# Kernel optimization log

Measured on AMD Instinct MI355X. Metric: run time of the kernel, lower is better.

The kernel has to match this reference:

```python
import jax, jax.numpy as jnp
import numpy as np

D_IN = 1024
D_OUT = 1024
NUM_HEADS = 16
HEAD_DIM = D_OUT // NUM_HEADS


def setup_inputs() -> dict:
    key = jax.random.key(0)
    ks = jax.random.split(key, 6)
    s = 0.02
    x = jax.random.normal(ks[0], (4, 2048, D_IN), dtype=jnp.float32)
    # nn.Linear weights are [out, in]
    Wq = jax.random.normal(ks[1], (D_OUT, D_IN), dtype=jnp.float32) * s
    Wk = jax.random.normal(ks[2], (D_OUT, D_IN), dtype=jnp.float32) * s
    Wv = jax.random.normal(ks[3], (D_OUT, D_IN), dtype=jnp.float32) * s
    Wo = jax.random.normal(ks[4], (D_OUT, D_OUT), dtype=jnp.float32) * s
    bo = jax.random.normal(ks[5], (D_OUT,), dtype=jnp.float32) * s
    return {"x": x, "Wq": Wq, "Wk": Wk, "Wv": Wv, "Wo": Wo, "bo": bo}


def reference(x, Wq, Wk, Wv, Wo, bo):
    B, T, _ = x.shape
    # project and split heads: [B, H, T, hd]
    def proj(W):
        return (x @ W.T).reshape(B, T, NUM_HEADS, HEAD_DIM).transpose(0, 2, 1, 3)
    q, k, v = proj(Wq), proj(Wk), proj(Wv)
    scores = jnp.einsum('bhqd,bhkd->bhqk', q, k) / jnp.sqrt(jnp.float32(HEAD_DIM))
    causal = jnp.tril(jnp.ones((T, T), dtype=bool))  # True = keep
    scores = jnp.where(causal, scores, -jnp.inf)
    attn = jax.nn.softmax(scores, axis=-1)
    ctx = jnp.einsum('bhqk,bhkd->bhqd', attn, v)  # [B,H,T,hd]
    ctx = ctx.transpose(0, 2, 1, 3).reshape(B, T, D_OUT)
    return ctx @ Wo.T + bo
```

## Files before the change

kernel.cpp:

```cpp
#include <hip/hip_runtime.h>

#define NH 16
#define HD 64
#define TSEQ 2048
#define DMODEL 1024

typedef __attribute__((ext_vector_type(8))) short short8;
typedef __attribute__((ext_vector_type(4))) float f32x4;

static __device__ __forceinline__ unsigned short f2bf(float f) {
    unsigned u = __builtin_bit_cast(unsigned, f);
    u += 0x7FFF + ((u >> 16) & 1);
    return (unsigned short)(u >> 16);
}

static __device__ __forceinline__ unsigned pk2(float a, float b) {
    unsigned ua = __builtin_bit_cast(unsigned, a);
    unsigned ub = __builtin_bit_cast(unsigned, b);
    return ((ua + 0x8000u) >> 16) | (((ub + 0x8000u) >> 16) << 16);
}

__global__ __launch_bounds__(256) void cast_f32_bf16(const float* __restrict__ src,
                                                     unsigned short* __restrict__ dst, int n4) {
    int i = blockIdx.x * 256 + threadIdx.x;
    if (i >= n4) return;
    float4 v = reinterpret_cast<const float4*>(src)[i];
    ushort4 o;
    o.x = f2bf(v.x); o.y = f2bf(v.y); o.z = f2bf(v.z); o.w = f2bf(v.w);
    reinterpret_cast<ushort4*>(dst)[i] = o;
}

static __device__ __forceinline__ void gemm_mainloop(const unsigned short* __restrict__ A,
                                                     const unsigned short* __restrict__ Bt,
                                                     int m0, int n0, int K,
                                                     unsigned short* As, unsigned short* Bs,
                                                     f32x4 acc[4][4]) {
    const int tid = threadIdx.x;
    const int lane = tid & 63;
    const int w = tid >> 6;
    const int wr = w >> 1, wc = w & 1;
    const int lrow = lane >> 2;
    const int lcol = (lane & 3) * 8;

    f32x4 zero = {0.f, 0.f, 0.f, 0.f};
#pragma unroll
    for (int i = 0; i < 4; i++)
#pragma unroll
        for (int j = 0; j < 4; j++) acc[i][j] = zero;

    for (int k0 = 0; k0 < K; k0 += 32) {
        __syncthreads();
#pragma unroll
        for (int c = w; c < 8; c += 4) {
            int row = c * 16 + lrow;
            __builtin_amdgcn_global_load_lds(
                (const __attribute__((address_space(1))) void*)(A + (size_t)(m0 + row) * K + k0 + lcol),
                (__attribute__((address_space(3))) void*)(As + c * 512), 16, 0, 0);
            __builtin_amdgcn_global_load_lds(
                (const __attribute__((address_space(1))) void*)(Bt + (size_t)(n0 + row) * K + k0 + lcol),
                (__attribute__((address_space(3))) void*)(Bs + c * 512), 16, 0, 0);
        }
        __syncthreads();

        const int ko = (lane >> 4) * 8;
        short8 a[4], b[4];
#pragma unroll
        for (int i = 0; i < 4; i++)
            a[i] = *(const short8*)(As + (wr * 64 + i * 16 + (lane & 15)) * 32 + ko);
#pragma unroll
        for (int j = 0; j < 4; j++)
            b[j] = *(const short8*)(Bs + (wc * 64 + j * 16 + (lane & 15)) * 32 + ko);
#pragma unroll
        for (int i = 0; i < 4; i++)
#pragma unroll
            for (int j = 0; j < 4; j++)
                acc[i][j] = __builtin_amdgcn_mfma_f32_16x16x32_bf16(a[i], b[j], acc[i][j], 0, 0, 0);
    }
}

#define QSCALE 0.180336880f
__global__ __launch_bounds__(256) void gemm_qkv(const unsigned short* __restrict__ xb,
                                                const unsigned short* __restrict__ Wqb,
                                                const unsigned short* __restrict__ Wkb,
                                                const unsigned short* __restrict__ Wvb,
                                                unsigned short* __restrict__ Q,
                                                unsigned short* __restrict__ K,
                                                unsigned short* __restrict__ Vt) {
    __shared__ __attribute__((aligned(16))) unsigned short As[128 * 32];
    __shared__ __attribute__((aligned(16))) unsigned short Bs[128 * 32];
    const int m0 = blockIdx.x * 128;
    const int n0 = blockIdx.y * 128;
    const int z = blockIdx.z;
    const unsigned short* Bt = (z == 0) ? Wqb : ((z == 1) ? Wkb : Wvb);
    unsigned short* out = (z == 0) ? Q : ((z == 1) ? K : Vt);

    f32x4 acc[4][4];
    gemm_mainloop(xb, Bt, m0, n0, DMODEL, As, Bs, acc);

    const int tid = threadIdx.x, lane = tid & 63, w = tid >> 6;
    const int wr = w >> 1, wc = w & 1;
    const float sc = (z == 0) ? QSCALE : 1.0f;
#pragma unroll
    for (int i = 0; i < 4; i++)
#pragma unroll
        for (int j = 0; j < 4; j++)
#pragma unroll
            for (int r = 0; r < 4; r++) {
                int row = m0 + wr * 64 + i * 16 + (lane >> 4) * 4 + r;
                int col = n0 + wc * 64 + j * 16 + (lane & 15);
                int b = row >> 11, t = row & 2047;
                int h = col >> 6, d = col & 63;
                unsigned short v = f2bf(acc[i][j][r] * sc);
                if (z == 2)
                    out[(((size_t)(b * NH + h)) * HD + d) * TSEQ + t] = v;
                else
                    out[(((size_t)(b * NH + h)) * TSEQ + t) * HD + d] = v;
            }
}

__global__ __launch_bounds__(256) void gemm_out(const unsigned short* __restrict__ ctx,
                                                const unsigned short* __restrict__ Wob,
                                                const float* __restrict__ bo,
                                                float* __restrict__ out) {
    __shared__ __attribute__((aligned(16))) unsigned short As[128 * 32];
    __shared__ __attribute__((aligned(16))) unsigned short Bs[128 * 32];
    const int m0 = blockIdx.x * 128;
    const int n0 = blockIdx.y * 128;

    f32x4 acc[4][4];
    gemm_mainloop(ctx, Wob, m0, n0, DMODEL, As, Bs, acc);

    const int tid = threadIdx.x, lane = tid & 63, w = tid >> 6;
    const int wr = w >> 1, wc = w & 1;
#pragma unroll
    for (int i = 0; i < 4; i++)
#pragma unroll
        for (int j = 0; j < 4; j++)
#pragma unroll
            for (int r = 0; r < 4; r++) {
                int row = m0 + wr * 64 + i * 16 + (lane >> 4) * 4 + r;
                int col = n0 + wc * 64 + j * 16 + (lane & 15);
                out[(size_t)row * DMODEL + col] = acc[i][j][r] + bo[col];
            }
}

__global__ __launch_bounds__(256) void attn(const unsigned short* __restrict__ Qg,
                                            const unsigned short* __restrict__ Kg,
                                            const unsigned short* __restrict__ Vg,
                                            unsigned short* __restrict__ ctx) {
    __shared__ __attribute__((aligned(16))) unsigned short Ks[64][72];
    __shared__ __attribute__((aligned(16))) unsigned short Vs[64][72];
    __shared__ __attribute__((aligned(16))) unsigned short Pl[128][76];

    const int tid = threadIdx.x, lane = tid & 63, w = tid >> 6;
    const int wq = w * 32;
    const int lg = lane >> 4;
    const int ll = lane & 15;
    const int bh = blockIdx.x;
    const int q0 = (gridDim.y - 1 - blockIdx.y) * 128;
    const unsigned short* Qh = Qg + (size_t)bh * TSEQ * HD;
    const unsigned short* Kh = Kg + (size_t)bh * TSEQ * HD;
    const unsigned short* Vh = Vg + (size_t)bh * HD * TSEQ;

    short8 qf[2][2];
#pragma unroll
    for (int rb = 0; rb < 2; rb++)
#pragma unroll
        for (int ks = 0; ks < 2; ks++)
            qf[rb][ks] = *(const short8*)(Qh + (size_t)(q0 + wq + rb * 16 + ll) * HD + ks * 32 + lg * 8);

    float mrun[2] = {-1e30f, -1e30f}, lrun[2] = {0.f, 0.f};
    f32x4 zero = {0.f, 0.f, 0.f, 0.f};
    f32x4 o_t[2][4];
#pragma unroll
    for (int rb = 0; rb < 2; rb++)
#pragma unroll
        for (int db = 0; db < 4; db++) o_t[rb][db] = zero;

    const int sr = tid >> 3;
    const int sc = (tid & 7) * 8;
    short8 kreg0, kreg1, vreg0, vreg1;
    {
        kreg0 = *(const short8*)(Kh + (size_t)(sr) * HD + sc);
        kreg1 = *(const short8*)(Kh + (size_t)(sr + 32) * HD + sc);
        vreg0 = *(const short8*)(Vh + (size_t)sr * TSEQ + sc);
        vreg1 = *(const short8*)(Vh + (size_t)(sr + 32) * TSEQ + sc);
    }

    const int nkv = q0 / 64 + 2;
    for (int kt = 0; kt < nkv; kt++) {
        const int kv0 = kt * 64;
        __builtin_amdgcn_s_barrier();
        __builtin_amdgcn_sched_barrier(0);
        *(short8*)&Ks[sr][sc] = kreg0;
        *(short8*)&Ks[sr + 32][sc] = kreg1;
        *(short8*)&Vs[sr][sc] = vreg0;
        *(short8*)&Vs[sr + 32][sc] = vreg1;
        if (kt + 1 < nkv) {
            const int nv0 = kv0 + 64;
            kreg0 = *(const short8*)(Kh + (size_t)(nv0 + sr) * HD + sc);
            kreg1 = *(const short8*)(Kh + (size_t)(nv0 + sr + 32) * HD + sc);
            vreg0 = *(const short8*)(Vh + (size_t)sr * TSEQ + nv0 + sc);
            vreg1 = *(const short8*)(Vh + (size_t)(sr + 32) * TSEQ + nv0 + sc);
        }
        __builtin_amdgcn_sched_barrier(0);
        asm volatile("s_waitcnt lgkmcnt(0)" ::: "memory");
        __builtin_amdgcn_s_barrier();
        __builtin_amdgcn_sched_barrier(0);

        f32x4 st[2][4];
#pragma unroll
        for (int rb = 0; rb < 2; rb++)
#pragma unroll
            for (int cb = 0; cb < 4; cb++) st[rb][cb] = zero;
#pragma unroll
        for (int ks = 0; ks < 2; ks++) {
            short8 afrag[4];
#pragma unroll
            for (int cb = 0; cb < 4; cb++)
                afrag[cb] = *(const short8*)&Ks[cb * 16 + ll][ks * 32 + lg * 8];
#pragma unroll
            for (int rb = 0; rb < 2; rb++)
#pragma unroll
                for (int cb = 0; cb < 4; cb++)
                    st[rb][cb] = __builtin_amdgcn_mfma_f32_16x16x32_bf16(afrag[cb], qf[rb][ks], st[rb][cb], 0, 0, 0);
        }

        if (kv0 + 63 > q0) {
#pragma unroll
            for (int rb = 0; rb < 2; rb++)
#pragma unroll
                for (int cb = 0; cb < 4; cb++)
#pragma unroll
                    for (int r = 0; r < 4; r++) {
                        int kvl = cb * 16 + lg * 4 + r;
                        int ql = wq + rb * 16 + ll;
                        if (kv0 + kvl > q0 + ql) st[rb][cb][r] = -1e30f;
                    }
        }

        float mx[2];
#pragma unroll
        for (int rb = 0; rb < 2; rb++) {
            float a0 = fmaxf(fmaxf(st[rb][0][0], st[rb][0][1]), fmaxf(st[rb][0][2], st[rb][0][3]));
            float a1 = fmaxf(fmaxf(st[rb][1][0], st[rb][1][1]), fmaxf(st[rb][1][2], st[rb][1][3]));
            float a2 = fmaxf(fmaxf(st[rb][2][0], st[rb][2][1]), fmaxf(st[rb][2][2], st[rb][2][3]));
            float a3 = fmaxf(fmaxf(st[rb][3][0], st[rb][3][1]), fmaxf(st[rb][3][2], st[rb][3][3]));
            float m = fmaxf(fmaxf(a0, a1), fmaxf(a2, a3));
            m = fmaxf(m, __shfl_xor(m, 16));
            m = fmaxf(m, __shfl_xor(m, 32));
            mx[rb] = m;
        }
        float need = fmaxf(mx[0] - mrun[0], mx[1] - mrun[1]);
        if (__any(need > 8.f)) {
#pragma unroll
            for (int rb = 0; rb < 2; rb++) {
                float mold = mrun[rb];
                float mn = fmaxf(mold, mx[rb]);
                float rs = __builtin_amdgcn_exp2f(mold - mn);
                mrun[rb] = mn;
                lrun[rb] *= rs;
#pragma unroll
                for (int db = 0; db < 4; db++)
#pragma unroll
                    for (int r = 0; r < 4; r++) o_t[rb][db][r] *= rs;
            }
        }
#pragma unroll
        for (int rb = 0; rb < 2; rb++) {
            float sum = 0.f;
#pragma unroll
            for (int cb = 0; cb < 4; cb++) {
                float p0 = __builtin_amdgcn_exp2f(st[rb][cb][0] - mrun[rb]);
                float p1 = __builtin_amdgcn_exp2f(st[rb][cb][1] - mrun[rb]);
                float p2 = __builtin_amdgcn_exp2f(st[rb][cb][2] - mrun[rb]);
                float p3 = __builtin_amdgcn_exp2f(st[rb][cb][3] - mrun[rb]);
                sum += (p0 + p1) + (p2 + p3);
                uint2 pw;
                pw.x = pk2(p0, p1);
                pw.y = pk2(p2, p3);
                *(uint2*)&Pl[wq + rb * 16 + ll][cb * 16 + lg * 4] = pw;
            }
            sum += __shfl_xor(sum, 16);
            sum += __shfl_xor(sum, 32);
            lrun[rb] += sum;
        }
        asm volatile("s_waitcnt lgkmcnt(0)" ::: "memory");
        __builtin_amdgcn_sched_barrier(0);

#pragma unroll
        for (int ks = 0; ks < 2; ks++) {
            short8 pa[2], va[4];
#pragma unroll
            for (int rb = 0; rb < 2; rb++)
                pa[rb] = *(const short8*)&Pl[wq + rb * 16 + ll][ks * 32 + lg * 8];
#pragma unroll
            for (int db = 0; db < 4; db++)
                va[db] = *(const short8*)&Vs[db * 16 + ll][ks * 32 + lg * 8];
#pragma unroll
            for (int rb = 0; rb < 2; rb++)
#pragma unroll
                for (int db = 0; db < 4; db++)
                    o_t[rb][db] = __builtin_amdgcn_mfma_f32_16x16x32_bf16(va[db], pa[rb], o_t[rb][db], 0, 0, 0);
        }
    }

    const int b = bh >> 4, h = bh & 15;
#pragma unroll
    for (int rb = 0; rb < 2; rb++) {
        float linv = 1.f / lrun[rb];
#pragma unroll
        for (int db = 0; db < 4; db++) {
            float v0 = o_t[rb][db][0] * linv, v1 = o_t[rb][db][1] * linv;
            float v2 = o_t[rb][db][2] * linv, v3 = o_t[rb][db][3] * linv;
            uint2 pw;
            pw.x = pk2(v0, v1);
            pw.y = pk2(v2, v3);
            *(uint2*)&Pl[wq + rb * 16 + ll][db * 16 + lg * 4] = pw;
        }
    }
    asm volatile("s_waitcnt lgkmcnt(0)" ::: "memory");
    __builtin_amdgcn_sched_barrier(0);
#pragma unroll
    for (int rb = 0; rb < 2; rb++)
#pragma unroll
        for (int half = 0; half < 2; half++) {
            short8 v = *(const short8*)&Pl[wq + rb * 16 + ll][half * 32 + lg * 8];
            size_t row = (size_t)(b * TSEQ + q0 + wq + rb * 16 + ll);
            *(short8*)(ctx + (row * NH + h) * HD + half * 32 + lg * 8) = v;
        }
}

extern "C" void kernel_launch(void* const* d_in, const int* in_sizes, int n_in,
                              void* d_out, int out_size, void* d_ws, size_t ws_size,
                              hipStream_t stream) {
    const float* x  = (const float*)d_in[0];
    const float* Wq = (const float*)d_in[1];
    const float* Wk = (const float*)d_in[2];
    const float* Wv = (const float*)d_in[3];
    const float* Wo = (const float*)d_in[4];
    const float* bo = (const float*)d_in[5];
    float* out = (float*)d_out;

    char* ws = (char*)d_ws;
    unsigned short* xb   = (unsigned short*)(ws);
    unsigned short* Wqb  = (unsigned short*)(ws + 16777216);
    unsigned short* Wkb  = (unsigned short*)(ws + 18874368);
    unsigned short* Wvb  = (unsigned short*)(ws + 20971520);
    unsigned short* Wob  = (unsigned short*)(ws + 23068672);
    unsigned short* Qb   = (unsigned short*)(ws + 25165824);
    unsigned short* Kb   = (unsigned short*)(ws + 41943040);
    unsigned short* Vtb  = (unsigned short*)(ws + 58720256);
    unsigned short* ctxb = (unsigned short*)(ws + 75497472);

    cast_f32_bf16<<<8192, 256, 0, stream>>>(x, xb, 2097152);
    cast_f32_bf16<<<1024, 256, 0, stream>>>(Wq, Wqb, 262144);
    cast_f32_bf16<<<1024, 256, 0, stream>>>(Wk, Wkb, 262144);
    cast_f32_bf16<<<1024, 256, 0, stream>>>(Wv, Wvb, 262144);
    cast_f32_bf16<<<1024, 256, 0, stream>>>(Wo, Wob, 262144);

    gemm_qkv<<<dim3(64, 8, 3), 256, 0, stream>>>(xb, Wqb, Wkb, Wvb, Qb, Kb, Vtb);
    attn<<<dim3(64, 16), 256, 0, stream>>>(Qb, Kb, Vtb, ctxb);
    gemm_out<<<dim3(64, 8), 256, 0, stream>>>(ctxb, Wob, bo, out);
}
```

Baseline: 204.8 us.

## Double-buffer GEMM LDS tiles, fuse weight casts, use hardware bf16 pack

The GEMM main loop now double-buffers its LDS tiles, issuing the async global-to-LDS load for the next K slice before computing on the current one, which cuts one barrier per iteration. The four weight-cast launches become a single kernel. In attention, the software bf16 rounding is replaced with the v_cvt_pk_bf16_f32 instruction, and the QK^T MFMA loop is reordered so all K fragments load first. The price is double the LDS per GEMM block, which may lower occupancy, and there is a possible race if the async LDS writes for the next slice are not waited on before the barrier.

```diff
diff --git a/kernel.cpp b/kernel.cpp
--- a/kernel.cpp
+++ b/kernel.cpp
@@ -14,10 +14,10 @@
     return (unsigned short)(u >> 16);
 }
 
-static __device__ __forceinline__ unsigned pk2(float a, float b) {
-    unsigned ua = __builtin_bit_cast(unsigned, a);
-    unsigned ub = __builtin_bit_cast(unsigned, b);
-    return ((ua + 0x8000u) >> 16) | (((ub + 0x8000u) >> 16) << 16);
+static __device__ __forceinline__ unsigned cvtpk(float a, float b) {
+    unsigned r;
+    asm("v_cvt_pk_bf16_f32 %0, %1, %2" : "=v"(r) : "v"(a), "v"(b));
+    return r;
 }
 
 __global__ __launch_bounds__(256) void cast_f32_bf16(const float* __restrict__ src,
@@ -28,6 +28,24 @@
     ushort4 o;
     o.x = f2bf(v.x); o.y = f2bf(v.y); o.z = f2bf(v.z); o.w = f2bf(v.w);
     reinterpret_cast<ushort4*>(dst)[i] = o;
+}
+
+__global__ __launch_bounds__(256) void cast_weights(const float* __restrict__ Wq,
+                                                    const float* __restrict__ Wk,
+                                                    const float* __restrict__ Wv,
+                                                    const float* __restrict__ Wo,
+                                                    unsigned short* __restrict__ dq,
+                                                    unsigned short* __restrict__ dk,
+                                                    unsigned short* __restrict__ dv,
+                                                    unsigned short* __restrict__ dwo) {
+    int g = blockIdx.x >> 10;
+    int i = (blockIdx.x & 1023) * 256 + threadIdx.x;
+    const float* s = (g == 0) ? Wq : (g == 1) ? Wk : (g == 2) ? Wv : Wo;
+    unsigned short* d = (g == 0) ? dq : (g == 1) ? dk : (g == 2) ? dv : dwo;
+    float4 v = reinterpret_cast<const float4*>(s)[i];
+    ushort4 o;
+    o.x = f2bf(v.x); o.y = f2bf(v.y); o.z = f2bf(v.z); o.w = f2bf(v.w);
+    reinterpret_cast<ushort4*>(d)[i] = o;
 }
 
 static __device__ __forceinline__ void gemm_mainloop(const unsigned short* __restrict__ A,
@@ -48,33 +66,41 @@
 #pragma unroll
         for (int j = 0; j < 4; j++) acc[i][j] = zero;
 
-    for (int k0 = 0; k0 < K; k0 += 32) {
-        __syncthreads();
+    auto stage = [&](int k0, int buf) {
 #pragma unroll
         for (int c = w; c < 8; c += 4) {
             int row = c * 16 + lrow;
             __builtin_amdgcn_global_load_lds(
                 (const __attribute__((address_space(1))) void*)(A + (size_t)(m0 + row) * K + k0 + lcol),
-                (__attribute__((address_space(3))) void*)(As + c * 512), 16, 0, 0);
+                (__attribute__((address_space(3))) void*)(As + buf * 4096 + c * 512), 16, 0, 0);
             __builtin_amdgcn_global_load_lds(
                 (const __attribute__((address_space(1))) void*)(Bt + (size_t)(n0 + row) * K + k0 + lcol),
-                (__attribute__((address_space(3))) void*)(Bs + c * 512), 16, 0, 0);
-        }
-        __syncthreads();
-
+                (__attribute__((address_space(3))) void*)(Bs + buf * 4096 + c * 512), 16, 0, 0);
+        }
+    };
+
+    stage(0, 0);
+    __syncthreads();
+    int cur = 0;
+    for (int k0 = 0; k0 < K; k0 += 32) {
+        if (k0 + 32 < K) stage(k0 + 32, cur ^ 1);
+        const unsigned short* Ab = As + cur * 4096;
+        const unsigned short* Bb = Bs + cur * 4096;
         const int ko = (lane >> 4) * 8;
         short8 a[4], b[4];
 #pragma unroll
         for (int i = 0; i < 4; i++)
-            a[i] = *(const short8*)(As + (wr * 64 + i * 16 + (lane & 15)) * 32 + ko);
+            a[i] = *(const short8*)(Ab + (wr * 64 + i * 16 + (lane & 15)) * 32 + ko);
 #pragma unroll
         for (int j = 0; j < 4; j++)
-            b[j] = *(const short8*)(Bs + (wc * 64 + j * 16 + (lane & 15)) * 32 + ko);
+            b[j] = *(const short8*)(Bb + (wc * 64 + j * 16 + (lane & 15)) * 32 + ko);
 #pragma unroll
         for (int i = 0; i < 4; i++)
 #pragma unroll
             for (int j = 0; j < 4; j++)
                 acc[i][j] = __builtin_amdgcn_mfma_f32_16x16x32_bf16(a[i], b[j], acc[i][j], 0, 0, 0);
+        __syncthreads();
+        cur ^= 1;
     }
 }
 
@@ -86,8 +112,8 @@
                                                 unsigned short* __restrict__ Q,
                                                 unsigned short* __restrict__ K,
                                                 unsigned short* __restrict__ Vt) {
-    __shared__ __attribute__((aligned(16))) unsigned short As[128 * 32];
-    __shared__ __attribute__((aligned(16))) unsigned short Bs[128 * 32];
+    __shared__ __attribute__((aligned(16))) unsigned short As[2 * 128 * 32];
+    __shared__ __attribute__((aligned(16))) unsigned short Bs[2 * 128 * 32];
     const int m0 = blockIdx.x * 128;
     const int n0 = blockIdx.y * 128;
     const int z = blockIdx.z;
@@ -122,8 +148,8 @@
                                                 const unsigned short* __restrict__ Wob,
                                                 const float* __restrict__ bo,
                                                 float* __restrict__ out) {
-    __shared__ __attribute__((aligned(16))) unsigned short As[128 * 32];
-    __shared__ __attribute__((aligned(16))) unsigned short Bs[128 * 32];
+    __shared__ __attribute__((aligned(16))) unsigned short As[2 * 128 * 32];
+    __shared__ __attribute__((aligned(16))) unsigned short Bs[2 * 128 * 32];
     const int m0 = blockIdx.x * 128;
     const int n0 = blockIdx.y * 128;
 
@@ -170,12 +196,12 @@
             qf[rb][ks] = *(const short8*)(Qh + (size_t)(q0 + wq + rb * 16 + ll) * HD + ks * 32 + lg * 8);
 
     float mrun[2] = {-1e30f, -1e30f}, lrun[2] = {0.f, 0.f};
-    f32x4 zero = {0.f, 0.f, 0.f, 0.f};
+    const f32x4 zerov = {0.f, 0.f, 0.f, 0.f};
     f32x4 o_t[2][4];
 #pragma unroll
     for (int rb = 0; rb < 2; rb++)
 #pragma unroll
-        for (int db = 0; db < 4; db++) o_t[rb][db] = zero;
+        for (int db = 0; db < 4; db++) o_t[rb][db] = zerov;
 
     const int sr = tid >> 3;
     const int sc = (tid & 7) * 8;
@@ -208,23 +234,23 @@
         __builtin_amdgcn_s_barrier();
         __builtin_amdgcn_sched_barrier(0);
 
+        short8 af0[4], af1[4];
+#pragma unroll
+        for (int cb = 0; cb < 4; cb++) {
+            af0[cb] = *(const short8*)&Ks[cb * 16 + ll][lg * 8];
+            af1[cb] = *(const short8*)&Ks[cb * 16 + ll][32 + lg * 8];
+        }
         f32x4 st[2][4];
 #pragma unroll
         for (int rb = 0; rb < 2; rb++)
 #pragma unroll
-            for (int cb = 0; cb < 4; cb++) st[rb][cb] = zero;
-#pragma unroll
-        for (int ks = 0; ks < 2; ks++) {
-            short8 afrag[4];
-#pragma unroll
             for (int cb = 0; cb < 4; cb++)
-                afrag[cb] = *(const short8*)&Ks[cb * 16 + ll][ks * 32 + lg * 8];
-#pragma unroll
-            for (int rb = 0; rb < 2; rb++)
-#pragma unroll
-                for (int cb = 0; cb < 4; cb++)
-                    st[rb][cb] = __builtin_amdgcn_mfma_f32_16x16x32_bf16(afrag[cb], qf[rb][ks], st[rb][cb], 0, 0, 0);
-        }
+                st[rb][cb] = __builtin_amdgcn_mfma_f32_16x16x32_bf16(af0[cb], qf[rb][0], zerov, 0, 0, 0);
+#pragma unroll
+        for (int rb = 0; rb < 2; rb++)
+#pragma unroll
+            for (int cb = 0; cb < 4; cb++)
+                st[rb][cb] = __builtin_amdgcn_mfma_f32_16x16x32_bf16(af1[cb], qf[rb][1], st[rb][cb], 0, 0, 0);
 
         if (kv0 + 63 > q0) {
 #pragma unroll
@@ -277,8 +303,8 @@
                 float p3 = __builtin_amdgcn_exp2f(st[rb][cb][3] - mrun[rb]);
                 sum += (p0 + p1) + (p2 + p3);
                 uint2 pw;
-                pw.x = pk2(p0, p1);
-                pw.y = pk2(p2, p3);
+                pw.x = cvtpk(p0, p1);
+                pw.y = cvtpk(p2, p3);
                 *(uint2*)&Pl[wq + rb * 16 + ll][cb * 16 + lg * 4] = pw;
             }
             sum += __shfl_xor(sum, 16);
@@ -311,11 +337,9 @@
         float linv = 1.f / lrun[rb];
 #pragma unroll
         for (int db = 0; db < 4; db++) {
-            float v0 = o_t[rb][db][0] * linv, v1 = o_t[rb][db][1] * linv;
-            float v2 = o_t[rb][db][2] * linv, v3 = o_t[rb][db][3] * linv;
             uint2 pw;
-            pw.x = pk2(v0, v1);
-            pw.y = pk2(v2, v3);
+            pw.x = cvtpk(o_t[rb][db][0] * linv, o_t[rb][db][1] * linv);
+            pw.y = cvtpk(o_t[rb][db][2] * linv, o_t[rb][db][3] * linv);
             *(uint2*)&Pl[wq + rb * 16 + ll][db * 16 + lg * 4] = pw;
         }
     }
@@ -354,10 +378,7 @@
     unsigned short* ctxb = (unsigned short*)(ws + 75497472);
 
     cast_f32_bf16<<<8192, 256, 0, stream>>>(x, xb, 2097152);
-    cast_f32_bf16<<<1024, 256, 0, stream>>>(Wq, Wqb, 262144);
-    cast_f32_bf16<<<1024, 256, 0, stream>>>(Wk, Wkb, 262144);
-    cast_f32_bf16<<<1024, 256, 0, stream>>>(Wv, Wvb, 262144);
-    cast_f32_bf16<<<1024, 256, 0, stream>>>(Wo, Wob, 262144);
+    cast_weights<<<4096, 256, 0, stream>>>(Wq, Wk, Wv, Wo, Wqb, Wkb, Wvb, Wob);
 
     gemm_qkv<<<dim3(64, 8, 3), 256, 0, stream>>>(xb, Wqb, Wkb, Wvb, Qb, Kb, Vtb);
     attn<<<dim3(64, 16), 256, 0, stream>>>(Qb, Kb, Vtb, ctxb);
```

Result: faster. 198.4 us (-3.1%).
